# Optimization experiments

Hardware: AMD Instinct MI355X
Metric: run time of the kernel (lower is better)

The kernel has to match this reference:

```python
import jax, jax.numpy as jnp
import numpy as np

# FlowNetC correlation config (matches init_kwargs)
PAD = 20          # pad_size
KERNEL = 1        # kernel_size (kernel_radius = 0)
MAX_DISP = 20     # max_displacement
STRIDE1 = 1       # output stride
STRIDE2 = 2       # displacement stride
RAD = MAX_DISP // STRIDE2   # neighborhood_grid_radius = 10 -> 21x21 = 441 displacements


def setup_inputs() -> dict:
    key = jax.random.key(0)
    k1, k2 = jax.random.split(key)
    B, C, H, W = 4, 256, 64, 96
    return {
        "input1": jax.random.normal(k1, (B, C, H, W), dtype=jnp.float32),
        "input2": jax.random.normal(k2, (B, C, H, W), dtype=jnp.float32),
    }


def reference(input1, input2):
    # input1, input2: [B, C, H, W]
    # Output: [B, (2*RAD+1)**2, H, W]  (pad_size == max_displacement, stride1 == 1,
    # kernel_size == 1 => output spatial size equals input spatial size).
    B, C, H, W = input1.shape
    p2 = jnp.pad(input2, ((0, 0), (0, 0), (PAD, PAD), (PAD, PAD)))
    norm = jnp.asarray(KERNEL * KERNEL * C, dtype=input1.dtype)
    outs = []
    # Fixed, small displacement grid (21x21): static slicing per displacement
    # avoids materializing a [441, B, C, H, W] intermediate.
    for dy in range(-RAD, RAD + 1):
        oy = PAD + dy * STRIDE2
        for dx in range(-RAD, RAD + 1):
            ox = PAD + dx * STRIDE2
            shifted = p2[:, :, oy:oy + H, ox:ox + W]        # [B, C, H, W]
            outs.append(jnp.sum(input1 * shifted, axis=1))  # [B, H, W]
    corr = jnp.stack(outs, axis=1) / norm                    # [B, 441, H, W]
    return corr
```

## Files before the change

### kernel.cpp

```cpp
#include <hip/hip_runtime.h>


typedef short bf16x8 __attribute__((ext_vector_type(8)));
typedef float f32x4  __attribute__((ext_vector_type(4)));

#define PLANE 24576
#define ST    40

__device__ __forceinline__ short f2bf(float f) {
    union { float f; unsigned u; } x; x.f = f;
    const unsigned u = x.u;
    return (short)((u + 0x7fffu + ((u >> 16) & 1u)) >> 16);
}

__global__ __launch_bounds__(512)
void corr_prepass(const float* __restrict__ in1, const float* __restrict__ in2,
                  short* __restrict__ dstA, short* __restrict__ dstB) {
    const int bid = blockIdx.x;
    const int sel = bid >> 8;
    const int r   = bid & 255;
    const int b   = r >> 6;
    const int yt  = (r >> 3) & 7;
    const int ct  = r & 7;
    const int c0 = ct * 32, y0 = yt * 8;
    const float* src = sel ? in2 : in1;
    short* dst = sel ? dstB : dstA;

    __shared__ __align__(16) short T[768 * ST];
    const int tid = threadIdx.x;

#pragma unroll
    for (int it = 0; it < 2; ++it) {
        const int d = it * 512 + tid;
        if (d < 768) {
            const int g = d / 192;
            const int f = d - g * 192;
            float4 v[8];
#pragma unroll
            for (int j = 0; j < 8; ++j) {
                const int c = c0 + g * 8 + j;
                v[j] = *(const float4*)(src + ((size_t)(b * 256 + c) * 64 + y0) * 96 + 4 * f);
            }
            bf16x8 w0, w1, w2, w3;
#pragma unroll
            for (int j = 0; j < 8; ++j) {
                w0[j] = f2bf(v[j].x); w1[j] = f2bf(v[j].y);
                w2[j] = f2bf(v[j].z); w3[j] = f2bf(v[j].w);
            }
            const int perm = ((g ^ (f & 3)) * 8);
            const int base = 4 * f * ST + perm;
            *(bf16x8*)&T[base]          = w0;
            *(bf16x8*)&T[base + ST]     = w1;
            *(bf16x8*)&T[base + 2*ST]   = w2;
            *(bf16x8*)&T[base + 3*ST]   = w3;
        }
    }
    __syncthreads();

#pragma unroll
    for (int it = 0; it < 6; ++it) {
        const int D  = it * 512 + tid;
        const int Rl = D >> 2, gp = D & 3;
        const int yy  = Rl / 96;
        const int rl  = Rl - yy * 96;
        const int par = rl / 48;
        const int col = rl - par * 48;
        const int x   = 2 * col + par;
        const int xx  = yy * 96 + x;
        const int perm = ((gp ^ ((xx >> 2) & 3)) * 8);
        const bf16x8 w = *(const bf16x8*)&T[xx * ST + perm];
        const size_t Rg = (size_t)(b * 64 + y0 + yy) * 96 + par * 48 + col;
        *(bf16x8*)(dst + Rg * 256 + c0 + gp * 8) = w;
    }
}

__global__ __launch_bounds__(512, 2)
void corr_mfma(const short* __restrict__ Ag, const short* __restrict__ Bg,
               float* __restrict__ out) {
    const int bhw = blockIdx.x;
    const int bid = ((bhw & 7) << 6) | (bhw >> 3);
    const int par = bid >> 8;
    const int b   = (bid >> 6) & 3;
    const int y2  = bid & 63;
    const int by2 = b * 64 + y2;

    const int tid  = threadIdx.x;
    const int lane = tid & 63, slot = tid >> 6;
    const int n    = lane & 15, q = lane >> 4;

    __shared__ __align__(16) short Bsh[48 * 256];
    __shared__ __align__(16) float scr[8][1008];

    {
        const short* src = Bg + (size_t)by2 * PLANE + par * 48 * 256;
#pragma unroll
        for (int it = 0; it < 3; ++it) {
            const int j   = it * 512 + tid;
            const int row = j >> 5;
            const int ofs = (row * 256 + (j & 31) * 8) ^ ((row & 7) << 3);
            *(bf16x8*)&Bsh[ofs] = *(const bf16x8*)(src + j * 8);
        }
    }
    __syncthreads();

    const bool v0 = (n >= 10), v3 = (n < 10);
    const int r0 = v0 ? (n - 10) : 0;
    const int r1 = n + 6;
    const int r2 = n + 22;
    const int r3 = v3 ? (n + 38) : 0;

    float* const sc = scr[slot];

#pragma unroll
    for (int p = 0; p < 3; ++p) {
        const int dyp = p * 8 + slot;
        const int y   = y2 + 20 - 2 * dyp;
        const bool live = (dyp < 21) && (y >= 0) && (y < 64);
        if (!live) continue;

        f32x4 acc[9];
#pragma unroll
        for (int t2 = 0; t2 < 9; ++t2) acc[t2] = (f32x4)0.0f;

        const short* Ap = Ag + ((size_t)(b * 64 + y) * 96 + par * 48) * 256
                        + n * 256 + q * 8;

        bf16x8 a0[3], a1[3], a2[3], a3[3];
#define LOADA(buf, ks) \
        buf[0] = *(const bf16x8*)(Ap + 0 * 4096 + (ks) * 32); \
        buf[1] = *(const bf16x8*)(Ap + 1 * 4096 + (ks) * 32); \
        buf[2] = *(const bf16x8*)(Ap + 2 * 4096 + (ks) * 32);

        LOADA(a0, 0) LOADA(a1, 1) LOADA(a2, 2) LOADA(a3, 3)

#define STEP(ks, ab, PF) { \
        const int ko = (ks) * 32 + q * 8; \
        bf16x8 b0 = *(const bf16x8*)&Bsh[(r0 * 256 + ko) ^ ((r0 & 7) << 3)]; if (!v0) b0 = 0; \
        bf16x8 b1 = *(const bf16x8*)&Bsh[(r1 * 256 + ko) ^ ((r1 & 7) << 3)]; \
        bf16x8 b2 = *(const bf16x8*)&Bsh[(r2 * 256 + ko) ^ ((r2 & 7) << 3)]; \
        bf16x8 b3 = *(const bf16x8*)&Bsh[(r3 * 256 + ko) ^ ((r3 & 7) << 3)]; if (!v3) b3 = 0; \
        acc[0] = __builtin_amdgcn_mfma_f32_16x16x32_bf16(ab[0], b0, acc[0], 0, 0, 0); \
        acc[1] = __builtin_amdgcn_mfma_f32_16x16x32_bf16(ab[0], b1, acc[1], 0, 0, 0); \
        acc[2] = __builtin_amdgcn_mfma_f32_16x16x32_bf16(ab[0], b2, acc[2], 0, 0, 0); \
        acc[3] = __builtin_amdgcn_mfma_f32_16x16x32_bf16(ab[1], b1, acc[3], 0, 0, 0); \
        acc[4] = __builtin_amdgcn_mfma_f32_16x16x32_bf16(ab[1], b2, acc[4], 0, 0, 0); \
        acc[5] = __builtin_amdgcn_mfma_f32_16x16x32_bf16(ab[1], b3, acc[5], 0, 0, 0); \
        acc[6] = __builtin_amdgcn_mfma_f32_16x16x32_bf16(ab[2], b2, acc[6], 0, 0, 0); \
        acc[7] = __builtin_amdgcn_mfma_f32_16x16x32_bf16(ab[2], b3, acc[7], 0, 0, 0); \
        if (PF) { LOADA(ab, (ks) + 4) } \
    }

        STEP(0, a0, 1) STEP(1, a1, 1) STEP(2, a2, 1) STEP(3, a3, 1)
        STEP(4, a0, 0) STEP(5, a1, 0) STEP(6, a2, 0) STEP(7, a3, 0)
#undef STEP
#undef LOADA

        const int mb = q * 4;
#pragma unroll
        for (int t2 = 0; t2 < 9; ++t2) {
            const int Xi = (t2 < 3) ? 0 : (t2 < 6 ? 1 : 2);
            constexpr int UJ[9] = {0, 1, 2, 1, 2, 3, 2, 3, 4};
            const int ub = UJ[t2] * 16;
#pragma unroll
            for (int rr = 0; rr < 4; ++rr) {
                const int xe = Xi * 16 + mb + rr;
                const int k  = ub + n - xe;
                if ((unsigned)k < 21u)
                    sc[xe * 21 + k] = acc[t2][rr];
            }
        }

        const size_t obase = ((size_t)(b * 441 + dyp * 21) * 64 + y) * 96 + par;
        float vals[16];
#pragma unroll
        for (int it = 0; it < 16; ++it) {
            const int e = it * 64 + lane;
            vals[it] = (e < 1008) ? sc[(e % 48) * 21 + (e / 48)] : 0.0f;
        }
#pragma unroll
        for (int it = 0; it < 16; ++it) {
            const int e = it * 64 + lane;
            if (e < 1008) {
                const int k  = e / 48;
                const int xe = e - k * 48;
                out[obase + (size_t)k * 6144 + 2 * xe] = vals[it] * (1.0f / 256.0f);
            }
        }
    }
}

extern "C" void kernel_launch(void* const* d_in, const int* in_sizes, int n_in,
                              void* d_out, int out_size, void* d_ws, size_t ws_size,
                              hipStream_t stream) {
    const float* in1 = (const float*)d_in[0];
    const float* in2 = (const float*)d_in[1];
    float* out = (float*)d_out;

    short* Ag = (short*)d_ws;
    short* Bg = Ag + (size_t)256 * PLANE;

    corr_prepass<<<dim3(512), dim3(512), 0, stream>>>(in1, in2, Ag, Bg);
    corr_mfma<<<dim3(512), dim3(512), 0, stream>>>(Ag, Bg, out);
}
```

Baseline: 134.1 us.

## Use inline-asm A loads with explicit vmcnt waits and remap block order

```diff
diff --git a/kernel.cpp b/kernel.cpp
--- a/kernel.cpp
+++ b/kernel.cpp
@@ -74,15 +74,26 @@
     }
 }
 
+#define GLOAD(dst, ptr, imm) \
+    asm volatile("global_load_dwordx4 %0, %1, off offset:%c2" \
+                 : "=&v"(dst) : "v"(ptr), "n"(imm))
+
+#define WAITV(N) \
+    asm volatile("s_waitcnt vmcnt(" #N ")"); \
+    __builtin_amdgcn_sched_barrier(0)
+
 __global__ __launch_bounds__(512, 2)
 void corr_mfma(const short* __restrict__ Ag, const short* __restrict__ Bg,
                float* __restrict__ out) {
     const int bhw = blockIdx.x;
     const int bid = ((bhw & 7) << 6) | (bhw >> 3);
-    const int par = bid >> 8;
-    const int b   = (bid >> 6) & 3;
-    const int y2  = bid & 63;
-    const int by2 = b * 64 + y2;
+    const int chunk = bid >> 6;
+    const int b    = chunk >> 1;
+    const int yhi  = chunk & 1;
+    const int inner = bid & 63;
+    const int par  = inner >> 5;
+    const int y2   = (yhi << 5) | (inner & 31);
+    const int by2  = b * 64 + y2;
 
     const int tid  = threadIdx.x;
     const int lane = tid & 63, slot = tid >> 6;
@@ -122,18 +133,20 @@
 #pragma unroll
         for (int t2 = 0; t2 < 9; ++t2) acc[t2] = (f32x4)0.0f;
 
-        const short* Ap = Ag + ((size_t)(b * 64 + y) * 96 + par * 48) * 256
-                        + n * 256 + q * 8;
+        const short* Ap  = Ag + ((size_t)(b * 64 + y) * 96 + par * 48) * 256
+                         + n * 256 + q * 8;
+        const short* ap0 = Ap;
+        const short* ap1 = Ap + 4096;
+        const short* ap2 = Ap + 8192;
 
         bf16x8 a0[3], a1[3], a2[3], a3[3];
-#define LOADA(buf, ks) \
-        buf[0] = *(const bf16x8*)(Ap + 0 * 4096 + (ks) * 32); \
-        buf[1] = *(const bf16x8*)(Ap + 1 * 4096 + (ks) * 32); \
-        buf[2] = *(const bf16x8*)(Ap + 2 * 4096 + (ks) * 32);
-
-        LOADA(a0, 0) LOADA(a1, 1) LOADA(a2, 2) LOADA(a3, 3)
-
-#define STEP(ks, ab, PF) { \
+        GLOAD(a0[0], ap0, 0);   GLOAD(a0[1], ap1, 0);   GLOAD(a0[2], ap2, 0);
+        GLOAD(a1[0], ap0, 64);  GLOAD(a1[1], ap1, 64);  GLOAD(a1[2], ap2, 64);
+        GLOAD(a2[0], ap0, 128); GLOAD(a2[1], ap1, 128); GLOAD(a2[2], ap2, 128);
+        GLOAD(a3[0], ap0, 192); GLOAD(a3[1], ap1, 192); GLOAD(a3[2], ap2, 192);
+
+#define STEP(ks, ab, NW, PF) { \
+        WAITV(NW); \
         const int ko = (ks) * 32 + q * 8; \
         bf16x8 b0 = *(const bf16x8*)&Bsh[(r0 * 256 + ko) ^ ((r0 & 7) << 3)]; if (!v0) b0 = 0; \
         bf16x8 b1 = *(const bf16x8*)&Bsh[(r1 * 256 + ko) ^ ((r1 & 7) << 3)]; \
@@ -147,13 +160,16 @@
         acc[5] = __builtin_amdgcn_mfma_f32_16x16x32_bf16(ab[1], b3, acc[5], 0, 0, 0); \
         acc[6] = __builtin_amdgcn_mfma_f32_16x16x32_bf16(ab[2], b2, acc[6], 0, 0, 0); \
         acc[7] = __builtin_amdgcn_mfma_f32_16x16x32_bf16(ab[2], b3, acc[7], 0, 0, 0); \
-        if (PF) { LOADA(ab, (ks) + 4) } \
-    }
-
-        STEP(0, a0, 1) STEP(1, a1, 1) STEP(2, a2, 1) STEP(3, a3, 1)
-        STEP(4, a0, 0) STEP(5, a1, 0) STEP(6, a2, 0) STEP(7, a3, 0)
+        if (PF) { \
+            GLOAD(ab[0], ap0, ((ks) + 4) * 64); \
+            GLOAD(ab[1], ap1, ((ks) + 4) * 64); \
+            GLOAD(ab[2], ap2, ((ks) + 4) * 64); \
+        } \
+    }
+
+        STEP(0, a0, 9, 1) STEP(1, a1, 9, 1) STEP(2, a2, 9, 1) STEP(3, a3, 9, 1)
+        STEP(4, a0, 9, 0) STEP(5, a1, 6, 0) STEP(6, a2, 3, 0) STEP(7, a3, 0, 0)
 #undef STEP
-#undef LOADA
 
         const int mb = q * 4;
 #pragma unroll
```

Result: no change. 135.8 us (+1.3%).

## Split displacement passes across blocks, halve scratch LDS, raise occupancy

Applied to the files above, without the earlier changes.

```diff
diff --git a/kernel.cpp b/kernel.cpp
--- a/kernel.cpp
+++ b/kernel.cpp
@@ -74,14 +74,18 @@
     }
 }
 
-__global__ __launch_bounds__(512, 2)
+__global__ __launch_bounds__(512, 3)
 void corr_mfma(const short* __restrict__ Ag, const short* __restrict__ Bg,
                float* __restrict__ out) {
     const int bhw = blockIdx.x;
-    const int bid = ((bhw & 7) << 6) | (bhw >> 3);
-    const int par = bid >> 8;
-    const int b   = (bid >> 6) & 3;
-    const int y2  = bid & 63;
+    const int xcd = bhw & 7;
+    const int i   = bhw >> 3;
+    const int b   = xcd >> 1;
+    const int yhi = xcd & 1;
+    const int p   = i >> 6;
+    const int rem = i & 63;
+    const int par = rem & 1;
+    const int y2  = (yhi << 5) | (rem >> 1);
     const int by2 = b * 64 + y2;
 
     const int tid  = threadIdx.x;
@@ -89,7 +93,7 @@
     const int n    = lane & 15, q = lane >> 4;
 
     __shared__ __align__(16) short Bsh[48 * 256];
-    __shared__ __align__(16) float scr[8][1008];
+    __shared__ __align__(16) float scr[8][528];
 
     {
         const short* src = Bg + (size_t)by2 * PLANE + par * 48 * 256;
@@ -103,6 +107,10 @@
     }
     __syncthreads();
 
+    const int dyp = p * 8 + slot;
+    const int y   = y2 + 20 - 2 * dyp;
+    if (dyp >= 21 || y < 0 || y >= 64) return;
+
     const bool v0 = (n >= 10), v3 = (n < 10);
     const int r0 = v0 ? (n - 10) : 0;
     const int r1 = n + 6;
@@ -111,51 +119,49 @@
 
     float* const sc = scr[slot];
 
-#pragma unroll
-    for (int p = 0; p < 3; ++p) {
-        const int dyp = p * 8 + slot;
-        const int y   = y2 + 20 - 2 * dyp;
-        const bool live = (dyp < 21) && (y >= 0) && (y < 64);
-        if (!live) continue;
-
-        f32x4 acc[9];
-#pragma unroll
-        for (int t2 = 0; t2 < 9; ++t2) acc[t2] = (f32x4)0.0f;
-
-        const short* Ap = Ag + ((size_t)(b * 64 + y) * 96 + par * 48) * 256
-                        + n * 256 + q * 8;
-
-        bf16x8 a0[3], a1[3], a2[3], a3[3];
+    f32x4 acc[9];
+#pragma unroll
+    for (int t2 = 0; t2 < 9; ++t2) acc[t2] = (f32x4)0.0f;
+
+    const short* Ap = Ag + ((size_t)(b * 64 + y) * 96 + par * 48) * 256
+                    + n * 256 + q * 8;
+
+    bf16x8 a0[3], a1[3], a2[3], a3[3];
 #define LOADA(buf, ks) \
-        buf[0] = *(const bf16x8*)(Ap + 0 * 4096 + (ks) * 32); \
-        buf[1] = *(const bf16x8*)(Ap + 1 * 4096 + (ks) * 32); \
-        buf[2] = *(const bf16x8*)(Ap + 2 * 4096 + (ks) * 32);
-
-        LOADA(a0, 0) LOADA(a1, 1) LOADA(a2, 2) LOADA(a3, 3)
+    buf[0] = *(const bf16x8*)(Ap + 0 * 4096 + (ks) * 32); \
+    buf[1] = *(const bf16x8*)(Ap + 1 * 4096 + (ks) * 32); \
+    buf[2] = *(const bf16x8*)(Ap + 2 * 4096 + (ks) * 32);
+
+    LOADA(a0, 0) LOADA(a1, 1) LOADA(a2, 2) LOADA(a3, 3)
 
 #define STEP(ks, ab, PF) { \
-        const int ko = (ks) * 32 + q * 8; \
-        bf16x8 b0 = *(const bf16x8*)&Bsh[(r0 * 256 + ko) ^ ((r0 & 7) << 3)]; if (!v0) b0 = 0; \
-        bf16x8 b1 = *(const bf16x8*)&Bsh[(r1 * 256 + ko) ^ ((r1 & 7) << 3)]; \
-        bf16x8 b2 = *(const bf16x8*)&Bsh[(r2 * 256 + ko) ^ ((r2 & 7) << 3)]; \
-        bf16x8 b3 = *(const bf16x8*)&Bsh[(r3 * 256 + ko) ^ ((r3 & 7) << 3)]; if (!v3) b3 = 0; \
-        acc[0] = __builtin_amdgcn_mfma_f32_16x16x32_bf16(ab[0], b0, acc[0], 0, 0, 0); \
-        acc[1] = __builtin_amdgcn_mfma_f32_16x16x32_bf16(ab[0], b1, acc[1], 0, 0, 0); \
-        acc[2] = __builtin_amdgcn_mfma_f32_16x16x32_bf16(ab[0], b2, acc[2], 0, 0, 0); \
-        acc[3] = __builtin_amdgcn_mfma_f32_16x16x32_bf16(ab[1], b1, acc[3], 0, 0, 0); \
-        acc[4] = __builtin_amdgcn_mfma_f32_16x16x32_bf16(ab[1], b2, acc[4], 0, 0, 0); \
-        acc[5] = __builtin_amdgcn_mfma_f32_16x16x32_bf16(ab[1], b3, acc[5], 0, 0, 0); \
-        acc[6] = __builtin_amdgcn_mfma_f32_16x16x32_bf16(ab[2], b2, acc[6], 0, 0, 0); \
-        acc[7] = __builtin_amdgcn_mfma_f32_16x16x32_bf16(ab[2], b3, acc[7], 0, 0, 0); \
-        if (PF) { LOADA(ab, (ks) + 4) } \
-    }
-
-        STEP(0, a0, 1) STEP(1, a1, 1) STEP(2, a2, 1) STEP(3, a3, 1)
-        STEP(4, a0, 0) STEP(5, a1, 0) STEP(6, a2, 0) STEP(7, a3, 0)
+    const int ko = (ks) * 32 + q * 8; \
+    bf16x8 b0 = *(const bf16x8*)&Bsh[(r0 * 256 + ko) ^ ((r0 & 7) << 3)]; if (!v0) b0 = 0; \
+    bf16x8 b1 = *(const bf16x8*)&Bsh[(r1 * 256 + ko) ^ ((r1 & 7) << 3)]; \
+    bf16x8 b2 = *(const bf16x8*)&Bsh[(r2 * 256 + ko) ^ ((r2 & 7) << 3)]; \
+    bf16x8 b3 = *(const bf16x8*)&Bsh[(r3 * 256 + ko) ^ ((r3 & 7) << 3)]; if (!v3) b3 = 0; \
+    acc[0] = __builtin_amdgcn_mfma_f32_16x16x32_bf16(ab[0], b0, acc[0], 0, 0, 0); \
+    acc[1] = __builtin_amdgcn_mfma_f32_16x16x32_bf16(ab[0], b1, acc[1], 0, 0, 0); \
+    acc[2] = __builtin_amdgcn_mfma_f32_16x16x32_bf16(ab[0], b2, acc[2], 0, 0, 0); \
+    acc[3] = __builtin_amdgcn_mfma_f32_16x16x32_bf16(ab[1], b1, acc[3], 0, 0, 0); \
+    acc[4] = __builtin_amdgcn_mfma_f32_16x16x32_bf16(ab[1], b2, acc[4], 0, 0, 0); \
+    acc[5] = __builtin_amdgcn_mfma_f32_16x16x32_bf16(ab[1], b3, acc[5], 0, 0, 0); \
+    acc[6] = __builtin_amdgcn_mfma_f32_16x16x32_bf16(ab[2], b2, acc[6], 0, 0, 0); \
+    acc[7] = __builtin_amdgcn_mfma_f32_16x16x32_bf16(ab[2], b3, acc[7], 0, 0, 0); \
+    if (PF) { LOADA(ab, (ks) + 4) } \
+}
+
+    STEP(0, a0, 1) STEP(1, a1, 1) STEP(2, a2, 1) STEP(3, a3, 1)
+    STEP(4, a0, 0) STEP(5, a1, 0) STEP(6, a2, 0) STEP(7, a3, 0)
 #undef STEP
 #undef LOADA
 
-        const int mb = q * 4;
+    const int mb = q * 4;
+#pragma unroll
+    for (int kp = 0; kp < 2; ++kp) {
+        const int k0 = kp ? 11 : 0;
+        const int kn = kp ? 10 : 11;
+
 #pragma unroll
         for (int t2 = 0; t2 < 9; ++t2) {
             const int Xi = (t2 < 3) ? 0 : (t2 < 6 ? 1 : 2);
@@ -165,25 +171,22 @@
             for (int rr = 0; rr < 4; ++rr) {
                 const int xe = Xi * 16 + mb + rr;
                 const int k  = ub + n - xe;
-                if ((unsigned)k < 21u)
-                    sc[xe * 21 + k] = acc[t2][rr];
-            }
-        }
-
-        const size_t obase = ((size_t)(b * 441 + dyp * 21) * 64 + y) * 96 + par;
-        float vals[16];
-#pragma unroll
-        for (int it = 0; it < 16; ++it) {
-            const int e = it * 64 + lane;
-            vals[it] = (e < 1008) ? sc[(e % 48) * 21 + (e / 48)] : 0.0f;
-        }
-#pragma unroll
-        for (int it = 0; it < 16; ++it) {
-            const int e = it * 64 + lane;
-            if (e < 1008) {
-                const int k  = e / 48;
-                const int xe = e - k * 48;
-                out[obase + (size_t)k * 6144 + 2 * xe] = vals[it] * (1.0f / 256.0f);
+                if ((unsigned)(k - k0) < (unsigned)kn)
+                    sc[xe * 11 + (k - k0)] = acc[t2][rr];
+            }
+        }
+
+        const size_t obase = ((size_t)(b * 441 + dyp * 21 + k0) * 64 + y) * 96 + par;
+        const int nit = kp ? 8 : 9;
+#pragma unroll
+        for (int it = 0; it < 9; ++it) {
+            if (it < nit) {
+                const int e = it * 64 + lane;
+                if (e < kn * 48) {
+                    const int k  = e / 48;
+                    const int xe = e - k * 48;
+                    out[obase + (size_t)k * 6144 + 2 * xe] = sc[xe * 11 + k] * (1.0f / 256.0f);
+                }
             }
         }
     }
@@ -200,5 +203,5 @@
     short* Bg = Ag + (size_t)256 * PLANE;
 
     corr_prepass<<<dim3(512), dim3(512), 0, stream>>>(in1, in2, Ag, Bg);
-    corr_mfma<<<dim3(512), dim3(512), 0, stream>>>(Ag, Bg, out);
-}
+    corr_mfma<<<dim3(1536), dim3(512), 0, stream>>>(Ag, Bg, out);
+}
```

Result: slower. 137.7 us (+2.7%).

## Pair two B rows per block so each A-row load feeds both displacement rows

Applied to the files above, without the earlier changes.

```diff
diff --git a/kernel.cpp b/kernel.cpp
--- a/kernel.cpp
+++ b/kernel.cpp
@@ -74,31 +74,52 @@
     }
 }
 
-__global__ __launch_bounds__(512, 2)
+#define GLOAD(dst, ptr, imm) \
+    asm volatile("global_load_dwordx4 %0, %1, off offset:%c2" \
+                 : "=&v"(dst) : "v"(ptr), "n"(imm) : "memory")
+#define WAITV0 \
+    asm volatile("s_waitcnt vmcnt(0)"); \
+    __builtin_amdgcn_sched_barrier(0)
+
+#define MFMA16(A, B, C) __builtin_amdgcn_mfma_f32_16x16x32_bf16(A, B, C, 0, 0, 0)
+
+__global__ __launch_bounds__(384, 3)
 void corr_mfma(const short* __restrict__ Ag, const short* __restrict__ Bg,
                float* __restrict__ out) {
     const int bhw = blockIdx.x;
     const int bid = ((bhw & 7) << 6) | (bhw >> 3);
-    const int par = bid >> 8;
-    const int b   = (bid >> 6) & 3;
-    const int y2  = bid & 63;
-    const int by2 = b * 64 + y2;
+    const int xcd = bid >> 6;
+    const int b   = xcd >> 1;
+    const int zhi = xcd & 1;
+    const int inner = bid & 63;
+    const int par = inner & 1;
+    const int z   = (zhi << 5) | (inner >> 1);
 
     const int tid  = threadIdx.x;
     const int lane = tid & 63, slot = tid >> 6;
     const int n    = lane & 15, q = lane >> 4;
 
-    __shared__ __align__(16) short Bsh[48 * 256];
-    __shared__ __align__(16) float scr[8][1008];
+    __shared__ __align__(16) short Bsh[2][48 * 256];
+    __shared__ __align__(16) float scr[6][528];
+
+    const int y2o = (z < 62) ? (z + 2) : (z - 62);
 
     {
-        const short* src = Bg + (size_t)by2 * PLANE + par * 48 * 256;
-#pragma unroll
-        for (int it = 0; it < 3; ++it) {
-            const int j   = it * 512 + tid;
+        const short* se = Bg + (size_t)(b * 64 + z)   * PLANE + par * 48 * 256;
+        const short* so = Bg + (size_t)(b * 64 + y2o) * PLANE + par * 48 * 256;
+#pragma unroll
+        for (int it = 0; it < 4; ++it) {
+            const int j   = it * 384 + tid;
             const int row = j >> 5;
             const int ofs = (row * 256 + (j & 31) * 8) ^ ((row & 7) << 3);
-            *(bf16x8*)&Bsh[ofs] = *(const bf16x8*)(src + j * 8);
+            *(bf16x8*)&Bsh[0][ofs] = *(const bf16x8*)(se + j * 8);
+        }
+#pragma unroll
+        for (int it = 0; it < 4; ++it) {
+            const int j   = it * 384 + tid;
+            const int row = j >> 5;
+            const int ofs = (row * 256 + (j & 31) * 8) ^ ((row & 7) << 3);
+            *(bf16x8*)&Bsh[1][ofs] = *(const bf16x8*)(so + j * 8);
         }
     }
     __syncthreads();
@@ -108,85 +129,117 @@
     const int r1 = n + 6;
     const int r2 = n + 22;
     const int r3 = v3 ? (n + 38) : 0;
-
     float* const sc = scr[slot];
 
-#pragma unroll
-    for (int p = 0; p < 3; ++p) {
-        const int dyp = p * 8 + slot;
-        const int y   = y2 + 20 - 2 * dyp;
-        const bool live = (dyp < 21) && (y >= 0) && (y < 64);
-        if (!live) continue;
-
-        f32x4 acc[9];
-#pragma unroll
-        for (int t2 = 0; t2 < 9; ++t2) acc[t2] = (f32x4)0.0f;
-
-        const short* Ap = Ag + ((size_t)(b * 64 + y) * 96 + par * 48) * 256
-                        + n * 256 + q * 8;
+#define STEPX(ks, ab, BS, AC) { \
+    const int ko = (ks) * 32 + q * 8; \
+    bf16x8 b0 = *(const bf16x8*)&BS[(r0 * 256 + ko) ^ ((r0 & 7) << 3)]; if (!v0) b0 = 0; \
+    bf16x8 b1 = *(const bf16x8*)&BS[(r1 * 256 + ko) ^ ((r1 & 7) << 3)]; \
+    bf16x8 b2 = *(const bf16x8*)&BS[(r2 * 256 + ko) ^ ((r2 & 7) << 3)]; \
+    bf16x8 b3 = *(const bf16x8*)&BS[(r3 * 256 + ko) ^ ((r3 & 7) << 3)]; if (!v3) b3 = 0; \
+    AC[0] = MFMA16(ab[0], b0, AC[0]); \
+    AC[1] = MFMA16(ab[0], b1, AC[1]); \
+    AC[2] = MFMA16(ab[0], b2, AC[2]); \
+    AC[3] = MFMA16(ab[1], b1, AC[3]); \
+    AC[4] = MFMA16(ab[1], b2, AC[4]); \
+    AC[5] = MFMA16(ab[1], b3, AC[5]); \
+    AC[6] = MFMA16(ab[2], b2, AC[6]); \
+    AC[7] = MFMA16(ab[2], b3, AC[7]); }
+
+#define GL12(P0, P1, P2, BASE) \
+    GLOAD(a0[0], P0, (BASE) + 0);   GLOAD(a0[1], P1, (BASE) + 0);   GLOAD(a0[2], P2, (BASE) + 0);   \
+    GLOAD(a1[0], P0, (BASE) + 64);  GLOAD(a1[1], P1, (BASE) + 64);  GLOAD(a1[2], P2, (BASE) + 64);  \
+    GLOAD(a2[0], P0, (BASE) + 128); GLOAD(a2[1], P1, (BASE) + 128); GLOAD(a2[2], P2, (BASE) + 128); \
+    GLOAD(a3[0], P0, (BASE) + 192); GLOAD(a3[1], P1, (BASE) + 192); GLOAD(a3[2], P2, (BASE) + 192);
+
+#define EPILOG(DYP, Y, AC) { \
+    const int mb = q * 4; \
+    _Pragma("unroll") \
+    for (int kp = 0; kp < 2; ++kp) { \
+        const int k0 = kp ? 11 : 0; \
+        const int kn = kp ? 10 : 11; \
+        _Pragma("unroll") \
+        for (int t2 = 0; t2 < 9; ++t2) { \
+            const int Xi = (t2 < 3) ? 0 : (t2 < 6 ? 1 : 2); \
+            constexpr int UJ[9] = {0, 1, 2, 1, 2, 3, 2, 3, 4}; \
+            const int ub = UJ[t2] * 16; \
+            _Pragma("unroll") \
+            for (int rr = 0; rr < 4; ++rr) { \
+                const int xe = Xi * 16 + mb + rr; \
+                const int k  = ub + n - xe; \
+                if ((unsigned)(k - k0) < (unsigned)kn) \
+                    sc[xe * 11 + (k - k0)] = AC[t2][rr]; \
+            } \
+        } \
+        const size_t ob = ((size_t)(b * 441 + (DYP) * 21 + k0) * 64 + (Y)) * 96 + par; \
+        const int nit = kp ? 8 : 9; \
+        _Pragma("unroll") \
+        for (int it2 = 0; it2 < 9; ++it2) { \
+            if (it2 < nit) { \
+                const int e = it2 * 64 + lane; \
+                if (e < kn * 48) { \
+                    const int k  = e / 48; \
+                    const int xe = e - k * 48; \
+                    out[ob + (size_t)k * 6144 + 2 * xe] = sc[xe * 11 + k] * (1.0f / 256.0f); \
+                } \
+            } \
+        } \
+    } }
+
+#pragma unroll
+    for (int p = 0; p < 2; ++p) {
+        const int m = p * 6 + slot;
+        if (m >= 11) continue;
+        const int dyp_e = 2 * m, dyp_o = 2 * m + 1;
+        const int y_e = z   + 20 - 4 * m;
+        const int y_o = y2o + 18 - 4 * m;
+        const bool live_e = (y_e >= 0) && (y_e < 64);
+        const bool live_o = (m < 10) && (y_o >= 0) && (y_o < 64);
+        if (!live_e && !live_o) continue;
+
+        const int  y_ld = live_e ? y_e : y_o;
+        const bool rld  = live_o && (y_o != y_ld);
+
+        const short* ApL = Ag + ((size_t)(b * 64 + y_ld) * 96 + par * 48) * 256
+                         + n * 256 + q * 8;
+        const short* l0 = ApL, *l1 = ApL + 4096, *l2 = ApL + 8192;
+        const short* ApO = Ag + ((size_t)(b * 64 + y_o) * 96 + par * 48) * 256
+                         + n * 256 + q * 8;
+        const short* o0 = ApO, *o1 = ApO + 4096, *o2 = ApO + 8192;
+
+        f32x4 accE[9], accO[9];
+#pragma unroll
+        for (int t = 0; t < 9; ++t) { accE[t] = (f32x4)0.0f; accO[t] = (f32x4)0.0f; }
 
         bf16x8 a0[3], a1[3], a2[3], a3[3];
-#define LOADA(buf, ks) \
-        buf[0] = *(const bf16x8*)(Ap + 0 * 4096 + (ks) * 32); \
-        buf[1] = *(const bf16x8*)(Ap + 1 * 4096 + (ks) * 32); \
-        buf[2] = *(const bf16x8*)(Ap + 2 * 4096 + (ks) * 32);
-
-        LOADA(a0, 0) LOADA(a1, 1) LOADA(a2, 2) LOADA(a3, 3)
-
-#define STEP(ks, ab, PF) { \
-        const int ko = (ks) * 32 + q * 8; \
-        bf16x8 b0 = *(const bf16x8*)&Bsh[(r0 * 256 + ko) ^ ((r0 & 7) << 3)]; if (!v0) b0 = 0; \
-        bf16x8 b1 = *(const bf16x8*)&Bsh[(r1 * 256 + ko) ^ ((r1 & 7) << 3)]; \
-        bf16x8 b2 = *(const bf16x8*)&Bsh[(r2 * 256 + ko) ^ ((r2 & 7) << 3)]; \
-        bf16x8 b3 = *(const bf16x8*)&Bsh[(r3 * 256 + ko) ^ ((r3 & 7) << 3)]; if (!v3) b3 = 0; \
-        acc[0] = __builtin_amdgcn_mfma_f32_16x16x32_bf16(ab[0], b0, acc[0], 0, 0, 0); \
-        acc[1] = __builtin_amdgcn_mfma_f32_16x16x32_bf16(ab[0], b1, acc[1], 0, 0, 0); \
-        acc[2] = __builtin_amdgcn_mfma_f32_16x16x32_bf16(ab[0], b2, acc[2], 0, 0, 0); \
-        acc[3] = __builtin_amdgcn_mfma_f32_16x16x32_bf16(ab[1], b1, acc[3], 0, 0, 0); \
-        acc[4] = __builtin_amdgcn_mfma_f32_16x16x32_bf16(ab[1], b2, acc[4], 0, 0, 0); \
-        acc[5] = __builtin_amdgcn_mfma_f32_16x16x32_bf16(ab[1], b3, acc[5], 0, 0, 0); \
-        acc[6] = __builtin_amdgcn_mfma_f32_16x16x32_bf16(ab[2], b2, acc[6], 0, 0, 0); \
-        acc[7] = __builtin_amdgcn_mfma_f32_16x16x32_bf16(ab[2], b3, acc[7], 0, 0, 0); \
-        if (PF) { LOADA(ab, (ks) + 4) } \
-    }
-
-        STEP(0, a0, 1) STEP(1, a1, 1) STEP(2, a2, 1) STEP(3, a3, 1)
-        STEP(4, a0, 0) STEP(5, a1, 0) STEP(6, a2, 0) STEP(7, a3, 0)
-#undef STEP
-#undef LOADA
-
-        const int mb = q * 4;
-#pragma unroll
-        for (int t2 = 0; t2 < 9; ++t2) {
-            const int Xi = (t2 < 3) ? 0 : (t2 < 6 ? 1 : 2);
-            constexpr int UJ[9] = {0, 1, 2, 1, 2, 3, 2, 3, 4};
-            const int ub = UJ[t2] * 16;
-#pragma unroll
-            for (int rr = 0; rr < 4; ++rr) {
-                const int xe = Xi * 16 + mb + rr;
-                const int k  = ub + n - xe;
-                if ((unsigned)k < 21u)
-                    sc[xe * 21 + k] = acc[t2][rr];
-            }
-        }
-
-        const size_t obase = ((size_t)(b * 441 + dyp * 21) * 64 + y) * 96 + par;
-        float vals[16];
-#pragma unroll
-        for (int it = 0; it < 16; ++it) {
-            const int e = it * 64 + lane;
-            vals[it] = (e < 1008) ? sc[(e % 48) * 21 + (e / 48)] : 0.0f;
-        }
-#pragma unroll
-        for (int it = 0; it < 16; ++it) {
-            const int e = it * 64 + lane;
-            if (e < 1008) {
-                const int k  = e / 48;
-                const int xe = e - k * 48;
-                out[obase + (size_t)k * 6144 + 2 * xe] = vals[it] * (1.0f / 256.0f);
-            }
-        }
-    }
+
+        GL12(l0, l1, l2, 0) WAITV0;
+        if (live_e) {
+            STEPX(0, a0, Bsh[0], accE) STEPX(1, a1, Bsh[0], accE)
+            STEPX(2, a2, Bsh[0], accE) STEPX(3, a3, Bsh[0], accE)
+        }
+        if (live_o) {
+            if (rld) { GL12(o0, o1, o2, 0) WAITV0; }
+            STEPX(0, a0, Bsh[1], accO) STEPX(1, a1, Bsh[1], accO)
+            STEPX(2, a2, Bsh[1], accO) STEPX(3, a3, Bsh[1], accO)
+        }
+        GL12(l0, l1, l2, 256) WAITV0;
+        if (live_e) {
+            STEPX(4, a0, Bsh[0], accE) STEPX(5, a1, Bsh[0], accE)
+            STEPX(6, a2, Bsh[0], accE) STEPX(7, a3, Bsh[0], accE)
+        }
+        if (live_o) {
+            if (rld) { GL12(o0, o1, o2, 256) WAITV0; }
+            STEPX(4, a0, Bsh[1], accO) STEPX(5, a1, Bsh[1], accO)
+            STEPX(6, a2, Bsh[1], accO) STEPX(7, a3, Bsh[1], accO)
+        }
+
+        if (live_e) EPILOG(dyp_e, y_e, accE)
+        if (live_o) EPILOG(dyp_o, y_o, accO)
+    }
+#undef STEPX
+#undef GL12
+#undef EPILOG
 }
 
 extern "C" void kernel_launch(void* const* d_in, const int* in_sizes, int n_in,
@@ -200,5 +253,5 @@
     short* Bg = Ag + (size_t)256 * PLANE;
 
     corr_prepass<<<dim3(512), dim3(512), 0, stream>>>(in1, in2, Ag, Bg);
-    corr_mfma<<<dim3(512), dim3(512), 0, stream>>>(Ag, Bg, out);
-}
+    corr_mfma<<<dim3(512), dim3(384), 0, stream>>>(Ag, Bg, out);
+}
```

After: 144.7 us. 7.9% more time.
